# Kernel tuning notes

Measured on AMD Instinct MI355X. Metric: run time of the kernel, lower is better.

Reference implementation:

```python
import jax, jax.numpy as jnp
import numpy as np

N_HEAD = 8
PREFIX_LEN = 77  # hardcoded text prefix length in the 'prefix' model_type branch
MASKED_BIAS = -10000.0


def setup_inputs() -> dict:
    key = jax.random.key(0)
    k1, k2, k3 = jax.random.split(key, 3)
    B, S, D = 8, 1024, 1024
    x = jax.random.normal(k1, (B, S, D), dtype=jnp.float32)
    attention_mask = jnp.zeros((B, 1, 1, S), dtype=jnp.float32)
    W_attn = jax.random.normal(k2, (D, 3 * D), dtype=jnp.float32) * 0.02
    b_attn = jnp.zeros((3 * D,), dtype=jnp.float32)
    W_proj = jax.random.normal(k3, (D, D), dtype=jnp.float32) * 0.02
    b_proj = jnp.zeros((D,), dtype=jnp.float32)
    return {"x": x, "attention_mask": attention_mask, "W_attn": W_attn,
            "b_attn": b_attn, "W_proj": W_proj, "b_proj": b_proj}


def _prefix_mask(S):
    # Rows < 77: attend only to cols < 77 (bidirectional prefix).
    # Rows >= 77: standard causal (cols <= row).
    row = jnp.arange(S)[:, None]
    col = jnp.arange(S)[None, :]
    return jnp.where(row < PREFIX_LEN, col < PREFIX_LEN, col <= row)  # [S, S] bool


def reference(x, attention_mask, W_attn, b_attn, W_proj, b_proj):
    B, S, D = x.shape
    H = N_HEAD
    hd = D // H
    qkv = x @ W_attn + b_attn                         # [B, S, 3D]
    q, k, v = jnp.split(qkv, 3, axis=-1)
    q = q.reshape(B, S, H, hd).transpose(0, 2, 1, 3)  # [B, H, S, hd]
    k = k.reshape(B, S, H, hd).transpose(0, 2, 1, 3)
    v = v.reshape(B, S, H, hd).transpose(0, 2, 1, 3)
    w = jnp.einsum('bhqd,bhkd->bhqk', q, k) / jnp.sqrt(jnp.float32(hd))
    mask = _prefix_mask(S)[None, None]                # [1, 1, S, S]
    w = jnp.where(mask, w, jnp.float32(MASKED_BIAS))
    w = w + attention_mask                            # additive mask [B,1,1,S]
    w = jax.nn.softmax(w, axis=-1)
    # dropout omitted (eval-mode reference)
    a = jnp.einsum('bhqk,bhkd->bhqd', w, v)           # [B, H, S, hd]
    a = a.transpose(0, 2, 1, 3).reshape(B, S, D)      # merge heads
    return a @ W_proj + b_proj
```

## Files before the change

### kernel.cpp

```cpp
#include <hip/hip_runtime.h>
#include <cstdint>
#include <cstddef>

#define B_  8
#define S_  1024
#define D_  1024
#define H_  8
#define HD_ 128
#define N3_ 3072
#define PREFIX 77
#define MASKED_BIAS -10000.0f

typedef __bf16 bf16x8 __attribute__((ext_vector_type(8)));
typedef float  f32x4  __attribute__((ext_vector_type(4)));

__device__ __forceinline__ unsigned short f2bf_rne(float f) {
    unsigned int u = __float_as_uint(f);
    u += 0x7FFFu + ((u >> 16) & 1u);
    return (unsigned short)(u >> 16);
}
__device__ __forceinline__ float bf2f(unsigned short h) {
    return __uint_as_float(((unsigned int)h) << 16);
}

__device__ __forceinline__ void load_lds16(const unsigned short* g, unsigned short* l) {
    __builtin_amdgcn_global_load_lds(
        (const __attribute__((address_space(1))) unsigned int*)g,
        (__attribute__((address_space(3))) unsigned int*)l,
        16, 0, 0);
}


__global__ void cvt_bf16(const float* __restrict__ in, unsigned short* __restrict__ out, int n4) {
    int i = blockIdx.x * blockDim.x + threadIdx.x;
    if (i >= n4) return;
    float4 v = reinterpret_cast<const float4*>(in)[i];
    ushort4 o;
    o.x = f2bf_rne(v.x); o.y = f2bf_rne(v.y); o.z = f2bf_rne(v.z); o.w = f2bf_rne(v.w);
    reinterpret_cast<ushort4*>(out)[i] = o;
}

__global__ void transpose_cvt(const float* __restrict__ in, unsigned short* __restrict__ out,
                              int R, int C) {
    __shared__ float tile[32][33];
    const int c0 = blockIdx.x * 32, r0 = blockIdx.y * 32;
    const int tx = threadIdx.x, ty = threadIdx.y;
    #pragma unroll
    for (int i = 0; i < 4; ++i)
        tile[ty + i * 8][tx] = in[(size_t)(r0 + ty + i * 8) * C + c0 + tx];
    __syncthreads();
    #pragma unroll
    for (int i = 0; i < 4; ++i)
        out[(size_t)(c0 + ty + i * 8) * R + r0 + tx] = f2bf_rne(tile[tx][ty + i * 8]);
}

__global__ void transpose_v(const unsigned short* __restrict__ v, unsigned short* __restrict__ vt) {
    __shared__ unsigned short tile[32][33];
    const int bh = blockIdx.z;
    const int d0 = blockIdx.x * 32, s0 = blockIdx.y * 32;
    const unsigned short* vi = v + (size_t)bh * S_ * HD_;
    unsigned short* vo = vt + (size_t)bh * S_ * HD_;
    const int tx = threadIdx.x, ty = threadIdx.y;
    #pragma unroll
    for (int i = 0; i < 4; ++i)
        tile[ty + i * 8][tx] = vi[(size_t)(s0 + ty + i * 8) * HD_ + d0 + tx];
    __syncthreads();
    #pragma unroll
    for (int i = 0; i < 4; ++i)
        vo[(size_t)(d0 + ty + i * 8) * S_ + s0 + tx] = tile[tx][ty + i * 8];
}

__global__ __launch_bounds__(256) void gemm_qkv(
    const unsigned short* __restrict__ xb,
    const unsigned short* __restrict__ wt,
    const float* __restrict__ bias,
    unsigned short* __restrict__ qb,
    unsigned short* __restrict__ kb,
    unsigned short* __restrict__ vb) {
    __shared__ unsigned short As[128 * 32];
    __shared__ unsigned short Bs[128 * 32];
    const int tid = threadIdx.x;
    const int bid = (int)blockIdx.x;
    const int xcd = bid & 7, l = bid >> 3;
    const int m0 = (xcd * 8 + (l & 7)) * 128;
    const int n0 = (l >> 3) * 128;
    const int w = tid >> 6, lane = tid & 63;
    const int wm = (w >> 1) * 64, wn = (w & 1) * 64;
    const int l15 = lane & 15, l4 = lane >> 4;
    const int sr = lane >> 2;
    const int sc8 = (lane & 3) * 8;
    const unsigned short* gA0 = xb + (size_t)(m0 + w * 32 + sr) * 1024 + sc8;
    const unsigned short* gA1 = gA0 + 16 * 1024;
    const unsigned short* gB0 = wt + (size_t)(n0 + w * 32 + sr) * 1024 + sc8;
    const unsigned short* gB1 = gB0 + 16 * 1024;
    unsigned short* lA0 = As + w * 1024;
    unsigned short* lA1 = lA0 + 512;
    unsigned short* lB0 = Bs + w * 1024;
    unsigned short* lB1 = lB0 + 512;
    f32x4 acc[4][4] = {};
    for (int kt = 0; kt < 32; ++kt) {
        const int k0 = kt * 32;
        __syncthreads();
        load_lds16(gA0 + k0, lA0);
        load_lds16(gA1 + k0, lA1);
        load_lds16(gB0 + k0, lB0);
        load_lds16(gB1 + k0, lB1);
        __syncthreads();
        bf16x8 af[4], bfr[4];
        #pragma unroll
        for (int i = 0; i < 4; ++i) {
            af[i]  = *(const bf16x8*)&As[(wm + i * 16 + l15) * 32 + l4 * 8];
            bfr[i] = *(const bf16x8*)&Bs[(wn + i * 16 + l15) * 32 + l4 * 8];
        }
        #pragma unroll
        for (int mi = 0; mi < 4; ++mi)
            #pragma unroll
            for (int ni = 0; ni < 4; ++ni)
                acc[mi][ni] = __builtin_amdgcn_mfma_f32_16x16x32_bf16(af[mi], bfr[ni], acc[mi][ni], 0, 0, 0);
    }
    #pragma unroll
    for (int mi = 0; mi < 4; ++mi) {
        #pragma unroll
        for (int ni = 0; ni < 4; ++ni) {
            const int col = n0 + wn + ni * 16 + l15;
            const float bv = bias[col];
            const int part = col >> 10;
            const int cidx = col & 1023;
            const int h = cidx >> 7, d = cidx & 127;
            unsigned short* dst = (part == 0) ? qb : ((part == 1) ? kb : vb);
            #pragma unroll
            for (int r = 0; r < 4; ++r) {
                const int row = m0 + wm + mi * 16 + l4 * 4 + r;
                const int b = row >> 10, s = row & 1023;
                dst[((size_t)(b * 8 + h) * 1024 + s) * 128 + d] = f2bf_rne(acc[mi][ni][r] + bv);
            }
        }
    }
}

__global__ __launch_bounds__(256, 2) void attn(
    const unsigned short* __restrict__ qb,
    const unsigned short* __restrict__ kb,
    const unsigned short* __restrict__ vt,
    const float* __restrict__ amask,
    unsigned short* __restrict__ ah,
    unsigned short* __restrict__ al) {
    __shared__ unsigned short Ks[2][64 * 128];
    __shared__ unsigned short Vs[128 * 64];
    __shared__ unsigned short P_lds[4][16 * 72];
    const int tid = threadIdx.x;
    const int w = tid >> 6, lane = tid & 63;
    const int l15 = lane & 15, l4 = lane >> 4;
    const int bidx = (int)blockIdx.x;
    const int qt = 15 - (bidx >> 6);
    const int h = bidx & 7, b = (bidx >> 3) & 7;
    const int bh = b * H_ + h;
    const unsigned short* Q = qb + (size_t)bh * S_ * HD_;
    const unsigned short* Kg = kb + (size_t)bh * S_ * HD_;
    const unsigned short* Vg = vt + (size_t)bh * S_ * HD_;
    unsigned short* pl = P_lds[w];
    const float L2E = 1.44269504088896341f;
    const float SCL = 0.08838834764831845f * L2E;
    const float M2  = 8.0f;

    const int q0 = qt * 64;
    const int q0w = q0 + w * 16;
    bf16x8 qf[4];
    #pragma unroll
    for (int s = 0; s < 4; ++s)
        qf[s] = *(const bf16x8*)(Q + (size_t)(q0w + l15) * 128 + s * 32 + l4 * 8);
    float lsum[4] = {0.f, 0.f, 0.f, 0.f};
    f32x4 o[8] = {};
    const int limit = (q0 + 64 > PREFIX) ? (q0 + 64) : PREFIX;
    const int nkt = (limit + 63) >> 6;

    const int kr = lane >> 4;
    const int kc = lane & 15;
    const int vr = lane >> 3;
    const int vc = lane & 7;

    #pragma unroll
    for (int j = 0; j < 4; ++j) {
        const int rl = w * 16 + j * 4 + kr;
        const int g = kc ^ (j * 4 + kr);
        load_lds16(Kg + (size_t)rl * 128 + g * 8, &Ks[0][(w * 16 + j * 4) * 128]);
    }

    for (int kt = 0; kt < nkt; ++kt) {
        const int kbase = kt * 64;
        const int cur = kt & 1;
        __syncthreads();
        if (kt + 1 < nkt) {
            const int kb2 = (kt + 1) * 64;
            #pragma unroll
            for (int j = 0; j < 4; ++j) {
                const int rl = w * 16 + j * 4 + kr;
                const int g = kc ^ (j * 4 + kr);
                load_lds16(Kg + (size_t)(kb2 + rl) * 128 + g * 8, &Ks[cur ^ 1][(w * 16 + j * 4) * 128]);
            }
        }
        #pragma unroll
        for (int j = 0; j < 4; ++j) {
            const int rv = w * 32 + j * 8 + vr;
            const int g = vc ^ vr;
            load_lds16(Vg + (size_t)rv * 1024 + kbase + g * 8, &Vs[(w * 32 + j * 8) * 64]);
        }
        const bool full = (kbase + 64 <= PREFIX) || (q0w >= PREFIX && kbase + 64 <= q0w);
        #pragma unroll
        for (int t = 0; t < 4; ++t) {
            f32x4 sa = {};
            #pragma unroll
            for (int s = 0; s < 4; ++s) {
                bf16x8 kf = *(const bf16x8*)&Ks[cur][(t * 16 + l15) * 128 + (((s * 4 + l4) ^ l15) * 8)];
                sa = __builtin_amdgcn_mfma_f32_16x16x32_bf16(qf[s], kf, sa, 0, 0, 0);
            }
            const int kcol = kbase + t * 16 + l15;
            const float am = fmaf(amask[b * S_ + kcol], L2E, -M2);
            float p[4];
            if (full) {
                #pragma unroll
                for (int r = 0; r < 4; ++r) p[r] = exp2f(fmaf(sa[r], SCL, am));
            } else {
                #pragma unroll
                for (int r = 0; r < 4; ++r) {
                    const int row = q0w + l4 * 4 + r;
                    const bool keep = (row < PREFIX) ? (kcol < PREFIX) : (kcol <= row);
                    const float e = exp2f(fmaf(sa[r], SCL, am));
                    p[r] = keep ? e : 0.f;
                }
            }
            #pragma unroll
            for (int r = 0; r < 4; ++r) {
                lsum[r] += p[r];
                pl[(l4 * 4 + r) * 72 + t * 16 + l15] = f2bf_rne(p[r]);
            }
        }
        bf16x8 pf0 = *(const bf16x8*)&pl[l15 * 72 + l4 * 8];
        bf16x8 pf1 = *(const bf16x8*)&pl[l15 * 72 + 32 + l4 * 8];
        __syncthreads();
        #pragma unroll
        for (int n = 0; n < 8; ++n) {
            bf16x8 vf = *(const bf16x8*)&Vs[(n * 16 + l15) * 64 + ((l4 ^ (l15 & 7)) * 8)];
            o[n] = __builtin_amdgcn_mfma_f32_16x16x32_bf16(pf0, vf, o[n], 0, 0, 0);
        }
        #pragma unroll
        for (int n = 0; n < 8; ++n) {
            bf16x8 vf = *(const bf16x8*)&Vs[(n * 16 + l15) * 64 + ((((4 + l4) ^ (l15 & 7))) * 8)];
            o[n] = __builtin_amdgcn_mfma_f32_16x16x32_bf16(pf1, vf, o[n], 0, 0, 0);
        }
    }
    float inv_l[4];
    #pragma unroll
    for (int r = 0; r < 4; ++r) {
        float sm = lsum[r];
        sm += __shfl_xor(sm, 1);
        sm += __shfl_xor(sm, 2);
        sm += __shfl_xor(sm, 4);
        sm += __shfl_xor(sm, 8);
        inv_l[r] = 1.0f / sm;
    }
    #pragma unroll
    for (int n = 0; n < 8; ++n) {
        const int d = n * 16 + l15;
        #pragma unroll
        for (int r = 0; r < 4; ++r) {
            const int s = q0w + l4 * 4 + r;
            const float val = o[n][r] * inv_l[r];
            const size_t idx = ((size_t)b * 1024 + s) * 1024 + h * 128 + d;
            unsigned short hv = f2bf_rne(val);
            ah[idx] = hv;
            al[idx] = f2bf_rne(val - bf2f(hv));
        }
    }
}

__global__ __launch_bounds__(256) void gemm_proj(
    const unsigned short* __restrict__ ahp,
    const unsigned short* __restrict__ alp,
    const unsigned short* __restrict__ wh,
    const float* __restrict__ bias,
    float* __restrict__ out) {
    __shared__ unsigned short As[128 * 32];
    __shared__ unsigned short Bs[128 * 32];
    const int tid = threadIdx.x;
    const int bid = (int)blockIdx.x;
    const int xcd = bid & 7, l = bid >> 3;
    const int m0 = (xcd * 8 + (l >> 3)) * 128;
    const int n0 = (l & 7) * 128;
    const int w = tid >> 6, lane = tid & 63;
    const int wm = (w >> 1) * 64, wn = (w & 1) * 64;
    const int l15 = lane & 15, l4 = lane >> 4;
    const int sr = lane >> 2;
    const int sc8 = (lane & 3) * 8;
    const size_t offA = (size_t)(m0 + w * 32 + sr) * 1024 + sc8;
    const size_t offB = (size_t)(n0 + w * 32 + sr) * 1024 + sc8;
    unsigned short* lA0 = As + w * 1024;
    unsigned short* lA1 = lA0 + 512;
    unsigned short* lB0 = Bs + w * 1024;
    unsigned short* lB1 = lB0 + 512;
    f32x4 acc[4][4] = {};
    for (int kt = 0; kt < 64; ++kt) {
        const int seg = kt >> 5;
        const int k0 = (kt & 31) * 32;
        const unsigned short* Ap = ((seg == 1) ? alp : ahp) + offA + k0;
        const unsigned short* Bp = wh + offB + k0;
        __syncthreads();
        load_lds16(Ap, lA0);
        load_lds16(Ap + 16 * 1024, lA1);
        load_lds16(Bp, lB0);
        load_lds16(Bp + 16 * 1024, lB1);
        __syncthreads();
        bf16x8 af[4], bfr[4];
        #pragma unroll
        for (int i = 0; i < 4; ++i) {
            af[i]  = *(const bf16x8*)&As[(wm + i * 16 + l15) * 32 + l4 * 8];
            bfr[i] = *(const bf16x8*)&Bs[(wn + i * 16 + l15) * 32 + l4 * 8];
        }
        #pragma unroll
        for (int mi = 0; mi < 4; ++mi)
            #pragma unroll
            for (int ni = 0; ni < 4; ++ni)
                acc[mi][ni] = __builtin_amdgcn_mfma_f32_16x16x32_bf16(af[mi], bfr[ni], acc[mi][ni], 0, 0, 0);
    }
    #pragma unroll
    for (int mi = 0; mi < 4; ++mi) {
        #pragma unroll
        for (int ni = 0; ni < 4; ++ni) {
            const int col = n0 + wn + ni * 16 + l15;
            const float bv = bias[col];
            #pragma unroll
            for (int r = 0; r < 4; ++r) {
                const int row = m0 + wm + mi * 16 + l4 * 4 + r;
                out[(size_t)row * 1024 + col] = acc[mi][ni][r] + bv;
            }
        }
    }
}

extern "C" void kernel_launch(void* const* d_in, const int* in_sizes, int n_in,
                              void* d_out, int out_size, void* d_ws, size_t ws_size,
                              hipStream_t stream) {
    const float* x      = (const float*)d_in[0];
    const float* amask  = (const float*)d_in[1];
    const float* W_attn = (const float*)d_in[2];
    const float* b_attn = (const float*)d_in[3];
    const float* W_proj = (const float*)d_in[4];
    const float* b_proj = (const float*)d_in[5];
    float* out = (float*)d_out;

    char* ws = (char*)d_ws;
    unsigned short* xb  = (unsigned short*)(ws);
    unsigned short* wta = (unsigned short*)(ws + 16777216);
    unsigned short* qb  = (unsigned short*)(ws + 23068672);
    unsigned short* kb2 = (unsigned short*)(ws + 39845888);
    unsigned short* vb  = (unsigned short*)(ws + 56623104);
    unsigned short* vtb = (unsigned short*)(ws + 73400320);
    unsigned short* ahi = (unsigned short*)(ws + 90177536);
    unsigned short* alo = (unsigned short*)(ws + 106954752);
    unsigned short* wph = (unsigned short*)(ws + 123731968);

    cvt_bf16<<<8192, 256, 0, stream>>>(x, xb, (B_ * S_ * D_) / 4);
    transpose_cvt<<<dim3(N3_ / 32, D_ / 32), dim3(32, 8), 0, stream>>>(W_attn, wta, D_, N3_);
    transpose_cvt<<<dim3(D_ / 32, D_ / 32), dim3(32, 8), 0, stream>>>(W_proj, wph, D_, D_);
    gemm_qkv<<<dim3(1536), 256, 0, stream>>>(xb, wta, b_attn, qb, kb2, vb);
    transpose_v<<<dim3(HD_ / 32, S_ / 32, B_ * H_), dim3(32, 8), 0, stream>>>(vb, vtb);
    attn<<<dim3(1024), 256, 0, stream>>>(qb, kb2, vtb, amask, ahi, alo);
    gemm_proj<<<dim3(512), 256, 0, stream>>>(ahi, alo, wph, b_proj, out);
}
```

Measured before the change: 261.6 us.

## Multi-stage pipelined GEMMs with 256x128 tiles, swizzled LDS and setprio

Rewrites both GEMM kernels to use 512-thread blocks computing 256x128 tiles and a 5-buffer LDS ring that prefetches 3 stages ahead. Explicit vmcnt waits and a single barrier per K-step replace the two __syncthreads, and an XOR swizzle on LDS chunks targets bank conflicts. MFMA issue is wrapped in s_setprio. This hides global-load latency and raises data reuse, but uses far more LDS (about 120KB per block), and correctness depends on the hand-counted vmcnt values.

```diff
diff --git a/kernel.cpp b/kernel.cpp
--- a/kernel.cpp
+++ b/kernel.cpp
@@ -70,59 +70,85 @@
         vo[(size_t)(d0 + ty + i * 8) * S_ + s0 + tx] = tile[tx][ty + i * 8];
 }
 
-__global__ __launch_bounds__(256) void gemm_qkv(
+
+#define QK_ASTR (256 * 32)
+#define QK_BSTR (128 * 32)
+
+__global__ __launch_bounds__(512, 2) void gemm_qkv(
     const unsigned short* __restrict__ xb,
     const unsigned short* __restrict__ wt,
     const float* __restrict__ bias,
     unsigned short* __restrict__ qb,
     unsigned short* __restrict__ kb,
     unsigned short* __restrict__ vb) {
-    __shared__ unsigned short As[128 * 32];
-    __shared__ unsigned short Bs[128 * 32];
+    __shared__ unsigned short As[5 * QK_ASTR];
+    __shared__ unsigned short Bs[5 * QK_BSTR];
     const int tid = threadIdx.x;
+    const int w = tid >> 6, lane = tid & 63;
     const int bid = (int)blockIdx.x;
     const int xcd = bid & 7, l = bid >> 3;
-    const int m0 = (xcd * 8 + (l & 7)) * 128;
-    const int n0 = (l >> 3) * 128;
-    const int w = tid >> 6, lane = tid & 63;
-    const int wm = (w >> 1) * 64, wn = (w & 1) * 64;
+    const int m0 = (xcd * 4 + (l & 3)) * 256;
+    const int n0 = (l >> 2) * 128;
+    const int wrow = w >> 1, wcol = w & 1;
     const int l15 = lane & 15, l4 = lane >> 4;
-    const int sr = lane >> 2;
-    const int sc8 = (lane & 3) * 8;
-    const unsigned short* gA0 = xb + (size_t)(m0 + w * 32 + sr) * 1024 + sc8;
+    const int srow = lane >> 2;
+    const int sg = ((lane & 3) ^ ((lane >> 3) & 3)) * 8;
+    const unsigned short* gA0 = xb + (size_t)(m0 + w * 32 + srow) * 1024 + sg;
     const unsigned short* gA1 = gA0 + 16 * 1024;
-    const unsigned short* gB0 = wt + (size_t)(n0 + w * 32 + sr) * 1024 + sc8;
-    const unsigned short* gB1 = gB0 + 16 * 1024;
-    unsigned short* lA0 = As + w * 1024;
-    unsigned short* lA1 = lA0 + 512;
-    unsigned short* lB0 = Bs + w * 1024;
-    unsigned short* lB1 = lB0 + 512;
+    const unsigned short* gB0 = wt + (size_t)(n0 + w * 16 + srow) * 1024 + sg;
+    unsigned short* lA = As + w * 1024;
+    unsigned short* lB = Bs + w * 512;
+    const int swz = (l15 >> 1) & 3;
+    const int ch8 = (l4 ^ swz) * 8;
+    int aoff[4], boff[4];
+    #pragma unroll
+    for (int i = 0; i < 4; ++i) {
+        aoff[i] = (wrow * 64 + i * 16 + l15) * 32 + ch8;
+        boff[i] = (wcol * 64 + i * 16 + l15) * 32 + ch8;
+    }
     f32x4 acc[4][4] = {};
-    for (int kt = 0; kt < 32; ++kt) {
-        const int k0 = kt * 32;
-        __syncthreads();
-        load_lds16(gA0 + k0, lA0);
-        load_lds16(gA1 + k0, lA1);
-        load_lds16(gB0 + k0, lB0);
-        load_lds16(gB1 + k0, lB1);
-        __syncthreads();
+
+    auto stage = [&](int tt, int sb) {
+        const int ko = tt * 32;
+        load_lds16(gA0 + ko, lA + sb * QK_ASTR);
+        load_lds16(gA1 + ko, lA + sb * QK_ASTR + 512);
+        load_lds16(gB0 + ko, lB + sb * QK_BSTR);
+    };
+    stage(0, 0); stage(1, 1); stage(2, 2);
+    int sbuf = 3, cbuf = 0;
+    for (int t = 0; t < 32; ++t) {
+        if (t <= 28) {
+            stage(t + 3, sbuf);
+            sbuf = (sbuf == 4) ? 0 : sbuf + 1;
+        }
+        if (t <= 28)      asm volatile("s_waitcnt vmcnt(9)" ::: "memory");
+        else if (t == 29) asm volatile("s_waitcnt vmcnt(6)" ::: "memory");
+        else if (t == 30) asm volatile("s_waitcnt vmcnt(3)" ::: "memory");
+        else              asm volatile("s_waitcnt vmcnt(0)" ::: "memory");
+        __builtin_amdgcn_s_barrier();
+        asm volatile("" ::: "memory");
+        const unsigned short* Ab = As + cbuf * QK_ASTR;
+        const unsigned short* Bb = Bs + cbuf * QK_BSTR;
+        cbuf = (cbuf == 4) ? 0 : cbuf + 1;
         bf16x8 af[4], bfr[4];
         #pragma unroll
         for (int i = 0; i < 4; ++i) {
-            af[i]  = *(const bf16x8*)&As[(wm + i * 16 + l15) * 32 + l4 * 8];
-            bfr[i] = *(const bf16x8*)&Bs[(wn + i * 16 + l15) * 32 + l4 * 8];
-        }
+            af[i]  = *(const bf16x8*)&Ab[aoff[i]];
+            bfr[i] = *(const bf16x8*)&Bb[boff[i]];
+        }
+        __builtin_amdgcn_s_setprio(1);
         #pragma unroll
         for (int mi = 0; mi < 4; ++mi)
             #pragma unroll
             for (int ni = 0; ni < 4; ++ni)
                 acc[mi][ni] = __builtin_amdgcn_mfma_f32_16x16x32_bf16(af[mi], bfr[ni], acc[mi][ni], 0, 0, 0);
+        __builtin_amdgcn_s_setprio(0);
     }
     #pragma unroll
     for (int mi = 0; mi < 4; ++mi) {
         #pragma unroll
         for (int ni = 0; ni < 4; ++ni) {
-            const int col = n0 + wn + ni * 16 + l15;
+            const int col = n0 + wcol * 64 + ni * 16 + l15;
             const float bv = bias[col];
             const int part = col >> 10;
             const int cidx = col & 1023;
@@ -130,7 +156,7 @@
             unsigned short* dst = (part == 0) ? qb : ((part == 1) ? kb : vb);
             #pragma unroll
             for (int r = 0; r < 4; ++r) {
-                const int row = m0 + wm + mi * 16 + l4 * 4 + r;
+                const int row = m0 + wrow * 64 + mi * 16 + l4 * 4 + r;
                 const int b = row >> 10, s = row & 1023;
                 dst[((size_t)(b * 8 + h) * 1024 + s) * 128 + d] = f2bf_rne(acc[mi][ni][r] + bv);
             }
@@ -274,63 +300,86 @@
     }
 }
 
-__global__ __launch_bounds__(256) void gemm_proj(
+__global__ __launch_bounds__(512, 2) void gemm_proj(
     const unsigned short* __restrict__ ahp,
     const unsigned short* __restrict__ alp,
     const unsigned short* __restrict__ wh,
     const float* __restrict__ bias,
     float* __restrict__ out) {
-    __shared__ unsigned short As[128 * 32];
-    __shared__ unsigned short Bs[128 * 32];
+    __shared__ unsigned short As[5 * QK_ASTR];
+    __shared__ unsigned short Bs[5 * QK_BSTR];
     const int tid = threadIdx.x;
+    const int w = tid >> 6, lane = tid & 63;
     const int bid = (int)blockIdx.x;
     const int xcd = bid & 7, l = bid >> 3;
-    const int m0 = (xcd * 8 + (l >> 3)) * 128;
-    const int n0 = (l & 7) * 128;
-    const int w = tid >> 6, lane = tid & 63;
-    const int wm = (w >> 1) * 64, wn = (w & 1) * 64;
+    const int m0 = (xcd * 4 + (l & 3)) * 256;
+    const int n0 = (l >> 2) * 128;
+    const int wrow = w >> 1, wcol = w & 1;
     const int l15 = lane & 15, l4 = lane >> 4;
-    const int sr = lane >> 2;
-    const int sc8 = (lane & 3) * 8;
-    const size_t offA = (size_t)(m0 + w * 32 + sr) * 1024 + sc8;
-    const size_t offB = (size_t)(n0 + w * 32 + sr) * 1024 + sc8;
-    unsigned short* lA0 = As + w * 1024;
-    unsigned short* lA1 = lA0 + 512;
-    unsigned short* lB0 = Bs + w * 1024;
-    unsigned short* lB1 = lB0 + 512;
+    const int srow = lane >> 2;
+    const int sg = ((lane & 3) ^ ((lane >> 3) & 3)) * 8;
+    const size_t offA = (size_t)(m0 + w * 32 + srow) * 1024 + sg;
+    const unsigned short* gAh = ahp + offA;
+    const unsigned short* gAl = alp + offA;
+    const unsigned short* gB0 = wh + (size_t)(n0 + w * 16 + srow) * 1024 + sg;
+    unsigned short* lA = As + w * 1024;
+    unsigned short* lB = Bs + w * 512;
+    const int swz = (l15 >> 1) & 3;
+    const int ch8 = (l4 ^ swz) * 8;
+    int aoff[4], boff[4];
+    #pragma unroll
+    for (int i = 0; i < 4; ++i) {
+        aoff[i] = (wrow * 64 + i * 16 + l15) * 32 + ch8;
+        boff[i] = (wcol * 64 + i * 16 + l15) * 32 + ch8;
+    }
     f32x4 acc[4][4] = {};
-    for (int kt = 0; kt < 64; ++kt) {
-        const int seg = kt >> 5;
-        const int k0 = (kt & 31) * 32;
-        const unsigned short* Ap = ((seg == 1) ? alp : ahp) + offA + k0;
-        const unsigned short* Bp = wh + offB + k0;
-        __syncthreads();
-        load_lds16(Ap, lA0);
-        load_lds16(Ap + 16 * 1024, lA1);
-        load_lds16(Bp, lB0);
-        load_lds16(Bp + 16 * 1024, lB1);
-        __syncthreads();
+
+    auto stage = [&](int tt, int sb) {
+        const int ko = (tt & 31) * 32;
+        const unsigned short* a = (tt < 32 ? gAh : gAl) + ko;
+        load_lds16(a, lA + sb * QK_ASTR);
+        load_lds16(a + 16 * 1024, lA + sb * QK_ASTR + 512);
+        load_lds16(gB0 + ko, lB + sb * QK_BSTR);
+    };
+    stage(0, 0); stage(1, 1); stage(2, 2);
+    int sbuf = 3, cbuf = 0;
+    for (int t = 0; t < 64; ++t) {
+        if (t <= 60) {
+            stage(t + 3, sbuf);
+            sbuf = (sbuf == 4) ? 0 : sbuf + 1;
+        }
+        if (t <= 60)      asm volatile("s_waitcnt vmcnt(9)" ::: "memory");
+        else if (t == 61) asm volatile("s_waitcnt vmcnt(6)" ::: "memory");
+        else if (t == 62) asm volatile("s_waitcnt vmcnt(3)" ::: "memory");
+        else              asm volatile("s_waitcnt vmcnt(0)" ::: "memory");
+        __builtin_amdgcn_s_barrier();
+        asm volatile("" ::: "memory");
+        const unsigned short* Ab = As + cbuf * QK_ASTR;
+        const unsigned short* Bb = Bs + cbuf * QK_BSTR;
+        cbuf = (cbuf == 4) ? 0 : cbuf + 1;
         bf16x8 af[4], bfr[4];
         #pragma unroll
         for (int i = 0; i < 4; ++i) {
-            af[i]  = *(const bf16x8*)&As[(wm + i * 16 + l15) * 32 + l4 * 8];
-            bfr[i] = *(const bf16x8*)&Bs[(wn + i * 16 + l15) * 32 + l4 * 8];
-        }
+            af[i]  = *(const bf16x8*)&Ab[aoff[i]];
+            bfr[i] = *(const bf16x8*)&Bb[boff[i]];
+        }
+        __builtin_amdgcn_s_setprio(1);
         #pragma unroll
         for (int mi = 0; mi < 4; ++mi)
             #pragma unroll
             for (int ni = 0; ni < 4; ++ni)
                 acc[mi][ni] = __builtin_amdgcn_mfma_f32_16x16x32_bf16(af[mi], bfr[ni], acc[mi][ni], 0, 0, 0);
+        __builtin_amdgcn_s_setprio(0);
     }
     #pragma unroll
     for (int mi = 0; mi < 4; ++mi) {
         #pragma unroll
         for (int ni = 0; ni < 4; ++ni) {
-            const int col = n0 + wn + ni * 16 + l15;
+            const int col = n0 + wcol * 64 + ni * 16 + l15;
             const float bv = bias[col];
             #pragma unroll
             for (int r = 0; r < 4; ++r) {
-                const int row = m0 + wm + mi * 16 + l4 * 4 + r;
+                const int row = m0 + wrow * 64 + mi * 16 + l4 * 4 + r;
                 out[(size_t)row * 1024 + col] = acc[mi][ni][r] + bv;
             }
         }
@@ -362,8 +411,8 @@
     cvt_bf16<<<8192, 256, 0, stream>>>(x, xb, (B_ * S_ * D_) / 4);
     transpose_cvt<<<dim3(N3_ / 32, D_ / 32), dim3(32, 8), 0, stream>>>(W_attn, wta, D_, N3_);
     transpose_cvt<<<dim3(D_ / 32, D_ / 32), dim3(32, 8), 0, stream>>>(W_proj, wph, D_, D_);
-    gemm_qkv<<<dim3(1536), 256, 0, stream>>>(xb, wta, b_attn, qb, kb2, vb);
+    gemm_qkv<<<dim3(768), 512, 0, stream>>>(xb, wta, b_attn, qb, kb2, vb);
     transpose_v<<<dim3(HD_ / 32, S_ / 32, B_ * H_), dim3(32, 8), 0, stream>>>(vb, vtb);
     attn<<<dim3(1024), 256, 0, stream>>>(qb, kb2, vtb, amask, ahi, alo);
-    gemm_proj<<<dim3(512), 256, 0, stream>>>(ahi, alo, wph, b_proj, out);
-}
+    gemm_proj<<<dim3(256), 512, 0, stream>>>(ahi, alo, wph, b_proj, out);
+}
```

New measurement: 268.8 us. +2.7%, slower.

## Double-buffer GEMM LDS tiles with XOR swizzle and merge prep kernels

Applied to the files above, without the earlier changes.

Both GEMMs now use two LDS buffers so the global-to-LDS load for the next k-tile is issued before the MFMA work on the current tile, leaving one barrier per iteration instead of two. Each lane's source column chunk is XOR-permuted with the matching permutation applied to the fragment reads, to reduce LDS bank conflicts. The fp32-to-bf16 conversion and the two weight transposes are merged into one launch to save launch overhead. The cost is doubled LDS per block, which may reduce occupancy.

```diff
diff --git a/kernel.cpp b/kernel.cpp
--- a/kernel.cpp
+++ b/kernel.cpp
@@ -30,28 +30,39 @@
         16, 0, 0);
 }
 
-
-__global__ void cvt_bf16(const float* __restrict__ in, unsigned short* __restrict__ out, int n4) {
-    int i = blockIdx.x * blockDim.x + threadIdx.x;
-    if (i >= n4) return;
-    float4 v = reinterpret_cast<const float4*>(in)[i];
-    ushort4 o;
-    o.x = f2bf_rne(v.x); o.y = f2bf_rne(v.y); o.z = f2bf_rne(v.z); o.w = f2bf_rne(v.w);
-    reinterpret_cast<ushort4*>(out)[i] = o;
-}
-
-__global__ void transpose_cvt(const float* __restrict__ in, unsigned short* __restrict__ out,
-                              int R, int C) {
+__global__ void prep(const float* __restrict__ x, unsigned short* __restrict__ xb,
+                     const float* __restrict__ Wa, unsigned short* __restrict__ wta,
+                     const float* __restrict__ Wp, unsigned short* __restrict__ wph) {
     __shared__ float tile[32][33];
-    const int c0 = blockIdx.x * 32, r0 = blockIdx.y * 32;
-    const int tx = threadIdx.x, ty = threadIdx.y;
+    const int bid = (int)blockIdx.x;
+    const int tid = threadIdx.x;
+    if (bid < 8192) {
+        const int i = bid * 256 + tid;
+        float4 v = reinterpret_cast<const float4*>(x)[i];
+        ushort4 o;
+        o.x = f2bf_rne(v.x); o.y = f2bf_rne(v.y); o.z = f2bf_rne(v.z); o.w = f2bf_rne(v.w);
+        reinterpret_cast<ushort4*>(xb)[i] = o;
+        return;
+    }
+    const float* in; unsigned short* out; int C, bx, by;
+    if (bid < 8192 + 3072) {
+        const int lb = bid - 8192;
+        in = Wa; out = wta; C = N3_;
+        bx = lb % 96; by = lb / 96;
+    } else {
+        const int lb = bid - 11264;
+        in = Wp; out = wph; C = D_;
+        bx = lb & 31; by = lb >> 5;
+    }
+    const int c0 = bx * 32, r0 = by * 32;
+    const int tx = tid & 31, ty = tid >> 5;
     #pragma unroll
     for (int i = 0; i < 4; ++i)
         tile[ty + i * 8][tx] = in[(size_t)(r0 + ty + i * 8) * C + c0 + tx];
     __syncthreads();
     #pragma unroll
     for (int i = 0; i < 4; ++i)
-        out[(size_t)(c0 + ty + i * 8) * R + r0 + tx] = f2bf_rne(tile[tx][ty + i * 8]);
+        out[(size_t)(c0 + ty + i * 8) * D_ + r0 + tx] = f2bf_rne(tile[tx][ty + i * 8]);
 }
 
 __global__ void transpose_v(const unsigned short* __restrict__ v, unsigned short* __restrict__ vt) {
@@ -77,8 +88,8 @@
     unsigned short* __restrict__ qb,
     unsigned short* __restrict__ kb,
     unsigned short* __restrict__ vb) {
-    __shared__ unsigned short As[128 * 32];
-    __shared__ unsigned short Bs[128 * 32];
+    __shared__ unsigned short As[2][128 * 32];
+    __shared__ unsigned short Bs[2][128 * 32];
     const int tid = threadIdx.x;
     const int bid = (int)blockIdx.x;
     const int xcd = bid & 7, l = bid >> 3;
@@ -87,36 +98,48 @@
     const int w = tid >> 6, lane = tid & 63;
     const int wm = (w >> 1) * 64, wn = (w & 1) * 64;
     const int l15 = lane & 15, l4 = lane >> 4;
-    const int sr = lane >> 2;
-    const int sc8 = (lane & 3) * 8;
-    const unsigned short* gA0 = xb + (size_t)(m0 + w * 32 + sr) * 1024 + sc8;
+    const int srow = lane >> 2;
+    const int sg = ((lane & 3) ^ ((lane >> 3) & 3)) * 8;
+    const unsigned short* gA0 = xb + (size_t)(m0 + w * 32 + srow) * 1024 + sg;
     const unsigned short* gA1 = gA0 + 16 * 1024;
-    const unsigned short* gB0 = wt + (size_t)(n0 + w * 32 + sr) * 1024 + sc8;
+    const unsigned short* gB0 = wt + (size_t)(n0 + w * 32 + srow) * 1024 + sg;
     const unsigned short* gB1 = gB0 + 16 * 1024;
-    unsigned short* lA0 = As + w * 1024;
-    unsigned short* lA1 = lA0 + 512;
-    unsigned short* lB0 = Bs + w * 1024;
-    unsigned short* lB1 = lB0 + 512;
+    const int ch8 = (l4 ^ ((l15 >> 1) & 3)) * 8;
+    int aoff[4], boff[4];
+    #pragma unroll
+    for (int i = 0; i < 4; ++i) {
+        aoff[i] = (wm + i * 16 + l15) * 32 + ch8;
+        boff[i] = (wn + i * 16 + l15) * 32 + ch8;
+    }
     f32x4 acc[4][4] = {};
+    auto stage = [&](int kt, int bi) {
+        const int k0 = kt * 32;
+        load_lds16(gA0 + k0, &As[bi][w * 1024]);
+        load_lds16(gA1 + k0, &As[bi][w * 1024 + 512]);
+        load_lds16(gB0 + k0, &Bs[bi][w * 1024]);
+        load_lds16(gB1 + k0, &Bs[bi][w * 1024 + 512]);
+    };
+    stage(0, 0);
+    asm volatile("s_waitcnt vmcnt(0)" ::: "memory");
+    __syncthreads();
     for (int kt = 0; kt < 32; ++kt) {
-        const int k0 = kt * 32;
-        __syncthreads();
-        load_lds16(gA0 + k0, lA0);
-        load_lds16(gA1 + k0, lA1);
-        load_lds16(gB0 + k0, lB0);
-        load_lds16(gB1 + k0, lB1);
-        __syncthreads();
+        const int cur = kt & 1;
+        if (kt < 31) stage(kt + 1, cur ^ 1);
         bf16x8 af[4], bfr[4];
         #pragma unroll
         for (int i = 0; i < 4; ++i) {
-            af[i]  = *(const bf16x8*)&As[(wm + i * 16 + l15) * 32 + l4 * 8];
-            bfr[i] = *(const bf16x8*)&Bs[(wn + i * 16 + l15) * 32 + l4 * 8];
+            af[i]  = *(const bf16x8*)&As[cur][aoff[i]];
+            bfr[i] = *(const bf16x8*)&Bs[cur][boff[i]];
         }
         #pragma unroll
         for (int mi = 0; mi < 4; ++mi)
             #pragma unroll
             for (int ni = 0; ni < 4; ++ni)
                 acc[mi][ni] = __builtin_amdgcn_mfma_f32_16x16x32_bf16(af[mi], bfr[ni], acc[mi][ni], 0, 0, 0);
+        if (kt < 31) {
+            asm volatile("s_waitcnt vmcnt(0)" ::: "memory");
+            __syncthreads();
+        }
     }
     #pragma unroll
     for (int mi = 0; mi < 4; ++mi) {
@@ -280,8 +303,8 @@
     const unsigned short* __restrict__ wh,
     const float* __restrict__ bias,
     float* __restrict__ out) {
-    __shared__ unsigned short As[128 * 32];
-    __shared__ unsigned short Bs[128 * 32];
+    __shared__ unsigned short As[2][128 * 32];
+    __shared__ unsigned short Bs[2][128 * 32];
     const int tid = threadIdx.x;
     const int bid = (int)blockIdx.x;
     const int xcd = bid & 7, l = bid >> 3;
@@ -290,37 +313,48 @@
     const int w = tid >> 6, lane = tid & 63;
     const int wm = (w >> 1) * 64, wn = (w & 1) * 64;
     const int l15 = lane & 15, l4 = lane >> 4;
-    const int sr = lane >> 2;
-    const int sc8 = (lane & 3) * 8;
-    const size_t offA = (size_t)(m0 + w * 32 + sr) * 1024 + sc8;
-    const size_t offB = (size_t)(n0 + w * 32 + sr) * 1024 + sc8;
-    unsigned short* lA0 = As + w * 1024;
-    unsigned short* lA1 = lA0 + 512;
-    unsigned short* lB0 = Bs + w * 1024;
-    unsigned short* lB1 = lB0 + 512;
+    const int srow = lane >> 2;
+    const int sg = ((lane & 3) ^ ((lane >> 3) & 3)) * 8;
+    const size_t offA = (size_t)(m0 + w * 32 + srow) * 1024 + sg;
+    const size_t offB = (size_t)(n0 + w * 32 + srow) * 1024 + sg;
+    const int ch8 = (l4 ^ ((l15 >> 1) & 3)) * 8;
+    int aoff[4], boff[4];
+    #pragma unroll
+    for (int i = 0; i < 4; ++i) {
+        aoff[i] = (wm + i * 16 + l15) * 32 + ch8;
+        boff[i] = (wn + i * 16 + l15) * 32 + ch8;
+    }
     f32x4 acc[4][4] = {};
+    auto stage = [&](int tt, int bi) {
+        const int k0 = (tt & 31) * 32;
+        const unsigned short* Ap = ((tt >> 5) ? alp : ahp) + offA + k0;
+        const unsigned short* Bp = wh + offB + k0;
+        load_lds16(Ap, &As[bi][w * 1024]);
+        load_lds16(Ap + 16 * 1024, &As[bi][w * 1024 + 512]);
+        load_lds16(Bp, &Bs[bi][w * 1024]);
+        load_lds16(Bp + 16 * 1024, &Bs[bi][w * 1024 + 512]);
+    };
+    stage(0, 0);
+    asm volatile("s_waitcnt vmcnt(0)" ::: "memory");
+    __syncthreads();
     for (int kt = 0; kt < 64; ++kt) {
-        const int seg = kt >> 5;
-        const int k0 = (kt & 31) * 32;
-        const unsigned short* Ap = ((seg == 1) ? alp : ahp) + offA + k0;
-        const unsigned short* Bp = wh + offB + k0;
-        __syncthreads();
-        load_lds16(Ap, lA0);
-        load_lds16(Ap + 16 * 1024, lA1);
-        load_lds16(Bp, lB0);
-        load_lds16(Bp + 16 * 1024, lB1);
-        __syncthreads();
+        const int cur = kt & 1;
+        if (kt < 63) stage(kt + 1, cur ^ 1);
         bf16x8 af[4], bfr[4];
         #pragma unroll
         for (int i = 0; i < 4; ++i) {
-            af[i]  = *(const bf16x8*)&As[(wm + i * 16 + l15) * 32 + l4 * 8];
-            bfr[i] = *(const bf16x8*)&Bs[(wn + i * 16 + l15) * 32 + l4 * 8];
+            af[i]  = *(const bf16x8*)&As[cur][aoff[i]];
+            bfr[i] = *(const bf16x8*)&Bs[cur][boff[i]];
         }
         #pragma unroll
         for (int mi = 0; mi < 4; ++mi)
             #pragma unroll
             for (int ni = 0; ni < 4; ++ni)
                 acc[mi][ni] = __builtin_amdgcn_mfma_f32_16x16x32_bf16(af[mi], bfr[ni], acc[mi][ni], 0, 0, 0);
+        if (kt < 63) {
+            asm volatile("s_waitcnt vmcnt(0)" ::: "memory");
+            __syncthreads();
+        }
     }
     #pragma unroll
     for (int mi = 0; mi < 4; ++mi) {
@@ -359,9 +393,7 @@
     unsigned short* alo = (unsigned short*)(ws + 106954752);
     unsigned short* wph = (unsigned short*)(ws + 123731968);
 
-    cvt_bf16<<<8192, 256, 0, stream>>>(x, xb, (B_ * S_ * D_) / 4);
-    transpose_cvt<<<dim3(N3_ / 32, D_ / 32), dim3(32, 8), 0, stream>>>(W_attn, wta, D_, N3_);
-    transpose_cvt<<<dim3(D_ / 32, D_ / 32), dim3(32, 8), 0, stream>>>(W_proj, wph, D_, D_);
+    prep<<<dim3(12288), 256, 0, stream>>>(x, xb, W_attn, wta, W_proj, wph);
     gemm_qkv<<<dim3(1536), 256, 0, stream>>>(xb, wta, b_attn, qb, kb2, vb);
     transpose_v<<<dim3(HD_ / 32, S_ / 32, B_ * H_), dim3(32, 8), 0, stream>>>(vb, vtb);
     attn<<<dim3(1024), 256, 0, stream>>>(qb, kb2, vtb, amask, ahi, alo);
```

Result: slower. 277.1 us (+5.9%).
